# Kernel tuning notes

Hardware: AMD Instinct MI355X
Metric: run time of the kernel (lower is better)

## Reference

```python
import jax, jax.numpy as jnp
import numpy as np

N = 50000
E = 800000
IN = 128
HID = 32
H1 = 8
H2 = 4
OUT = 64
D1 = HID * H1  # 256
D2 = HID * H2  # 128
NEG_SLOPE = 0.2


def _lin(key, fin, fout):
    k1, k2 = jax.random.split(key)
    s = 1.0 / np.sqrt(fin)
    W = jax.random.uniform(k1, (fin, fout), minval=-s, maxval=s, dtype=jnp.float32)
    b = jax.random.uniform(k2, (fout,), minval=-s, maxval=s, dtype=jnp.float32)
    return W, b


def setup_inputs() -> dict:
    key = jax.random.key(0)
    ks = jax.random.split(key, 24)
    x = jax.random.normal(ks[0], (N, IN), dtype=jnp.float32)
    edge_index = jax.random.randint(ks[1], (2, E), 0, N, dtype=jnp.int64)
    W_tr, b_tr = _lin(ks[2], IN, D1)
    # GAT1: D1 -> HID per head, H1 heads (concat)
    W1, _ = _lin(ks[3], D1, H1 * HID)
    as1 = jax.random.normal(ks[4], (H1, HID), dtype=jnp.float32) * 0.1
    ad1 = jax.random.normal(ks[5], (H1, HID), dtype=jnp.float32) * 0.1
    b1 = jnp.zeros((H1 * HID,), dtype=jnp.float32)
    # GRU1: h_dim=D1, h_in_dim=D1
    Wr1, br1 = _lin(ks[6], 2 * D1, D1)
    Wz1, bz1 = _lin(ks[7], 2 * D1, D1)
    Wh1, bh1 = _lin(ks[8], 2 * D1, D1)
    Wp2, bp2 = _lin(ks[9], D1, D2)
    # GAT2: D1 -> HID per head, H2 heads
    W2, _ = _lin(ks[10], D1, H2 * HID)
    as2 = jax.random.normal(ks[11], (H2, HID), dtype=jnp.float32) * 0.1
    ad2 = jax.random.normal(ks[12], (H2, HID), dtype=jnp.float32) * 0.1
    b2 = jnp.zeros((H2 * HID,), dtype=jnp.float32)
    # GRU2: h_dim=D2, h_in_dim=D2
    Wr2, br2 = _lin(ks[13], 2 * D2, D2)
    Wz2, bz2 = _lin(ks[14], 2 * D2, D2)
    Wh2, bh2 = _lin(ks[15], 2 * D2, D2)
    Wp3, bp3 = _lin(ks[16], D2, OUT)
    # GAT3: D2 -> OUT, 1 head
    W3, _ = _lin(ks[17], D2, OUT)
    as3 = jax.random.normal(ks[18], (1, OUT), dtype=jnp.float32) * 0.1
    ad3 = jax.random.normal(ks[19], (1, OUT), dtype=jnp.float32) * 0.1
    b3 = jnp.zeros((OUT,), dtype=jnp.float32)
    # GRU3
    Wr3, br3 = _lin(ks[20], 2 * OUT, OUT)
    Wz3, bz3 = _lin(ks[21], 2 * OUT, OUT)
    Wh3, bh3 = _lin(ks[22], 2 * OUT, OUT)
    return dict(x=x, edge_index=edge_index, W_tr=W_tr, b_tr=b_tr,
                W1=W1, as1=as1, ad1=ad1, b1=b1, Wr1=Wr1, br1=br1, Wz1=Wz1, bz1=bz1, Wh1=Wh1, bh1=bh1,
                Wp2=Wp2, bp2=bp2, W2=W2, as2=as2, ad2=ad2, b2=b2, Wr2=Wr2, br2=br2, Wz2=Wz2, bz2=bz2, Wh2=Wh2, bh2=bh2,
                Wp3=Wp3, bp3=bp3, W3=W3, as3=as3, ad3=ad3, b3=b3, Wr3=Wr3, br3=br3, Wz3=Wz3, bz3=bz3, Wh3=Wh3, bh3=bh3)


def gat_conv(x, src, dst, W, a_src, a_dst, bias, heads, out_ch):
    """PyG GATConv (concat=True, add_self_loops handled by caller, eval mode so no dropout)."""
    n = x.shape[0]
    xp = (x @ W).reshape(n, heads, out_ch)            # [N,H,C]
    alpha_s = (xp * a_src[None]).sum(-1)              # [N,H]
    alpha_d = (xp * a_dst[None]).sum(-1)              # [N,H]
    e = jax.nn.leaky_relu(alpha_s[src] + alpha_d[dst], NEG_SLOPE)  # [E,H]
    # segment softmax over incoming edges of each dst node
    emax = jax.ops.segment_max(e, dst, num_segments=n)
    e = jnp.exp(e - emax[dst])
    denom = jax.ops.segment_sum(e, dst, num_segments=n)
    alpha = e / (denom[dst] + 1e-16)                  # [E,H]
    msg = xp[src] * alpha[..., None]                  # [E,H,C]
    out = jax.ops.segment_sum(msg, dst, num_segments=n)
    return out.reshape(n, heads * out_ch) + bias


def gru_sub(h, h_in, Wr, br, Wz, bz, Wh, bh):
    a = jnp.concatenate([h, h_in], axis=1)
    r = jax.nn.sigmoid(a @ Wr + br)
    z = jax.nn.sigmoid(a @ Wz + bz)
    joined = jnp.concatenate([h, r * h_in], axis=1)
    h_hat = jnp.tanh(joined @ Wh + bh)
    return (1 - z) * h_in + z * h_hat


def reference(x, edge_index, W_tr, b_tr,
              W1, as1, ad1, b1, Wr1, br1, Wz1, bz1, Wh1, bh1,
              Wp2, bp2, W2, as2, ad2, b2, Wr2, br2, Wz2, bz2, Wh2, bh2,
              Wp3, bp3, W3, as3, ad3, b3, Wr3, br3, Wz3, bz3, Wh3, bh3):
    n = x.shape[0]
    # PyG GATConv adds self-loops by default
    loop = jnp.arange(n, dtype=edge_index.dtype)
    src = jnp.concatenate([edge_index[0], loop])
    dst = jnp.concatenate([edge_index[1], loop])

    x = x @ W_tr + b_tr                                # transform: IN -> D1
    h1 = x
    x = jax.nn.elu(gat_conv(x, src, dst, W1, as1, ad1, b1, H1, HID))
    x = gru_sub(x, h1, Wr1, br1, Wz1, bz1, Wh1, bh1)
    h2 = x
    x = jax.nn.elu(gat_conv(x, src, dst, W2, as2, ad2, b2, H2, HID))
    x = gru_sub(x, h2 @ Wp2 + bp2, Wr2, br2, Wz2, bz2, Wh2, bh2)
    h3 = x
    x = gat_conv(x, src, dst, W3, as3, ad3, b3, 1, OUT)
    x = gru_sub(x, h3 @ Wp3 + bp3, Wr3, br3, Wz3, bz3, Wh3, bh3)
    return x
```

## Files before the change

### kernel.cpp

```cpp
#include <hip/hip_runtime.h>

#define NEG_SLOPE 0.2f

typedef __attribute__((ext_vector_type(8))) short short8;
typedef __attribute__((ext_vector_type(8))) unsigned short ushort8;
typedef __attribute__((ext_vector_type(4))) float f32x4;

__device__ __forceinline__ unsigned short f2bf(float f) {
    unsigned int u = __float_as_uint(f);
    u += 0x7fff + ((u >> 16) & 1);
    return (unsigned short)(u >> 16);
}
__device__ __forceinline__ float bf2f(unsigned short s) {
    return __uint_as_float(((unsigned int)s) << 16);
}

__device__ __forceinline__ void gll16(const void* g, void* l) {
    __builtin_amdgcn_global_load_lds(
        (const __attribute__((address_space(1))) void*)g,
        (__attribute__((address_space(3))) void*)l, 16, 0, 0);
}

__global__ void conv_k(const float* __restrict__ in, unsigned short* __restrict__ out, long n)
{
    long i = ((long)blockIdx.x * blockDim.x + threadIdx.x) * 4;
    if (i >= n) return;
    float4 f = *(const float4*)&in[i];
    ushort4 o; o.x = f2bf(f.x); o.y = f2bf(f.y); o.z = f2bf(f.z); o.w = f2bf(f.w);
    *(ushort4*)&out[i] = o;
}

struct WPack {
    const float* W[15];
    unsigned short* Wc[15];
    int K[15];
    int MoS[15];
    int MoD[15];
    int off[15];
};
__global__ void convW_all(WPack p)
{
    int wi = blockIdx.y;
    int i = blockIdx.x * blockDim.x + threadIdx.x;
    int K = p.K[wi], MoS = p.MoS[wi];
    if (i >= K * MoS) return;
    int k = i / MoS, m = i % MoS;
    p.Wc[wi][((long)(k >> 3) * p.MoD[wi] + p.off[wi] + m) * 8 + (k & 7)] = f2bf(p.W[wi][i]);
}

__device__ __forceinline__ int xcd_work(int TOT) {
    int L = blockIdx.x;
    int per = (TOT + 7) >> 3;
    int wk = (L & 7) * per + (L >> 3);
    return (wk < TOT) ? wk : -1;
}

template<int BN, int MODE>
__global__ __launch_bounds__(256) void gemm_t(
    const unsigned short* __restrict__ U, int K1,
    const unsigned short* __restrict__ V, int K2,
    const unsigned short* __restrict__ Wc, const float* __restrict__ bias,
    float* __restrict__ outF, unsigned short* __restrict__ outB,
    unsigned short* __restrict__ outB2,
    const unsigned short* __restrict__ HinB, const unsigned short* __restrict__ Zb,
    const float* __restrict__ HinF, const float* __restrict__ Zf,
    int rows, int Mo)
{
    constexpr int NIF = BN / 32;
    __shared__ __align__(16) unsigned short As[8][64][8];
    __shared__ __align__(16) unsigned short Bs[8][BN][8];
    const int CB = Mo / BN;
    const int RB = (rows + 63) >> 6;
    int wk = xcd_work(CB * RB);
    if (wk < 0) return;
    const int col0 = (wk % CB) * BN;
    const int row0 = (wk / CB) * 64;
    const int K = K1 + K2;
    const int tid = threadIdx.x;
    const int l = tid & 63, w = tid >> 6;
    const int lm = l & 15, lg = l >> 4;
    const int wrow = (w >> 1) * 32;
    const int wcol = (w & 1) * (BN / 2);
    f32x4 acc[2][NIF] = {};

    for (int k0 = 0; k0 < K; k0 += 64) {
#pragma unroll
        for (int i = 0; i < 2; ++i) {
            int c = i * 256 + tid;
            int m = c & 63, g = c >> 6;
            int row = row0 + m; if (row >= rows) row = rows - 1;
            int k = k0 + g * 8;
            const unsigned short* sp = (k < K1) ? U + (long)row * K1 + k
                                                : V + (long)row * K2 + (k - K1);
            gll16(sp, &As[0][0][0] + ((i * 256 + w * 64) << 3));
        }
#pragma unroll
        for (int j = 0; j < NIF; ++j) {
            int c = j * 256 + tid;
            int n = c & (BN - 1), g = c / BN;
            gll16(Wc + ((long)((k0 >> 3) + g) * Mo + (col0 + n)) * 8,
                  &Bs[0][0][0] + ((j * 256 + w * 64) << 3));
        }
        __syncthreads();
#pragma unroll
        for (int kk = 0; kk < 2; ++kk) {
            short8 a[2], b[NIF];
#pragma unroll
            for (int mi = 0; mi < 2; ++mi)
                a[mi] = *(const short8*)&As[kk * 4 + lg][wrow + mi * 16 + lm][0];
#pragma unroll
            for (int ni = 0; ni < NIF; ++ni)
                b[ni] = *(const short8*)&Bs[kk * 4 + lg][wcol + ni * 16 + lm][0];
#pragma unroll
            for (int mi = 0; mi < 2; ++mi)
#pragma unroll
                for (int ni = 0; ni < NIF; ++ni)
                    acc[mi][ni] = __builtin_amdgcn_mfma_f32_16x16x32_bf16(a[mi], b[ni], acc[mi][ni], 0, 0, 0);
        }
        __syncthreads();
    }

    const int halfMo = Mo >> 1;
#pragma unroll
    for (int mi = 0; mi < 2; ++mi) {
        int rbase = row0 + wrow + mi * 16 + lg * 4;
#pragma unroll
        for (int r = 0; r < 4; ++r) {
            int row = rbase + r;
            if (row >= rows) continue;
#pragma unroll
            for (int ni = 0; ni < NIF; ++ni) {
                int col = col0 + wcol + ni * 16 + lm;
                float v = acc[mi][ni][r];
                if (MODE == 0) {
                    v += (bias ? bias[col] : 0.f);
                    long idx = (long)row * Mo + col;
                    if (outF) outF[idx] = v;
                    if (outB) outB[idx] = f2bf(v);
                } else if (MODE == 3) {
                    v += bias[col];
                    long idx = (long)row * Mo + col;
                    float z = bf2f(Zb[idx]);
                    float o = (1.f - z) * bf2f(HinB[idx]) + z * tanhf(v);
                    outB[idx] = f2bf(o);
                } else if (MODE == 5) {
                    v += bias[col];
                    long idx = (long)row * Mo + col;
                    float z = Zf[idx];
                    float o = (1.f - z) * HinF[idx] + z * tanhf(v);
                    outF[idx] = o;
                } else {
                    if (col < halfMo) {
                        v += bias[col];
                        long idx = (long)row * halfMo + col;
                        if (outF) outF[idx] = v;
                        outB[idx] = f2bf(v);
                    } else {
                        outB2[(long)row * halfMo + (col - halfMo)] = f2bf(v);
                    }
                }
            }
        }
    }
}

template<int FP>
__global__ __launch_bounds__(256) void gemm_rz(
    const unsigned short* __restrict__ U, int K1,
    const unsigned short* __restrict__ V, int K2,
    const unsigned short* __restrict__ Wrc, const unsigned short* __restrict__ Wzc,
    const float* __restrict__ br, const float* __restrict__ bz,
    const unsigned short* __restrict__ HinB, const float* __restrict__ HinF,
    unsigned short* __restrict__ RHb,
    unsigned short* __restrict__ ZoutB, float* __restrict__ ZoutF,
    int rows, int Mo)
{
    __shared__ __align__(16) unsigned short As[8][64][8];
    __shared__ __align__(16) unsigned short Br[8][64][8];
    __shared__ __align__(16) unsigned short Bz[8][64][8];
    const int CB = Mo >> 6;
    const int RB = (rows + 63) >> 6;
    int wk = xcd_work(CB * RB);
    if (wk < 0) return;
    const int col0 = (wk % CB) * 64;
    const int row0 = (wk / CB) * 64;
    const int K = K1 + K2;
    const int tid = threadIdx.x;
    const int l = tid & 63, w = tid >> 6;
    const int lm = l & 15, lg = l >> 4;
    const int wrow = (w >> 1) * 32;
    const int wcol = (w & 1) * 32;
    f32x4 accr[2][2] = {}, accz[2][2] = {};

    for (int k0 = 0; k0 < K; k0 += 64) {
#pragma unroll
        for (int i = 0; i < 2; ++i) {
            int c = i * 256 + tid;
            int m = c & 63, g = c >> 6;
            int row = row0 + m; if (row >= rows) row = rows - 1;
            int k = k0 + g * 8;
            const unsigned short* sp = (k < K1) ? U + (long)row * K1 + k
                                                : V + (long)row * K2 + (k - K1);
            gll16(sp, &As[0][0][0] + ((i * 256 + w * 64) << 3));
        }
#pragma unroll
        for (int j = 0; j < 2; ++j) {
            int c = j * 256 + tid;
            int n = c & 63, g = c >> 6;
            long base = ((long)((k0 >> 3) + g) * Mo + (col0 + n)) * 8;
            gll16(Wrc + base, &Br[0][0][0] + ((j * 256 + w * 64) << 3));
            gll16(Wzc + base, &Bz[0][0][0] + ((j * 256 + w * 64) << 3));
        }
        __syncthreads();
#pragma unroll
        for (int kk = 0; kk < 2; ++kk) {
            short8 a[2], brv[2], bzv[2];
#pragma unroll
            for (int mi = 0; mi < 2; ++mi)
                a[mi] = *(const short8*)&As[kk * 4 + lg][wrow + mi * 16 + lm][0];
#pragma unroll
            for (int ni = 0; ni < 2; ++ni) {
                brv[ni] = *(const short8*)&Br[kk * 4 + lg][wcol + ni * 16 + lm][0];
                bzv[ni] = *(const short8*)&Bz[kk * 4 + lg][wcol + ni * 16 + lm][0];
            }
#pragma unroll
            for (int mi = 0; mi < 2; ++mi)
#pragma unroll
                for (int ni = 0; ni < 2; ++ni) {
                    accr[mi][ni] = __builtin_amdgcn_mfma_f32_16x16x32_bf16(a[mi], brv[ni], accr[mi][ni], 0, 0, 0);
                    accz[mi][ni] = __builtin_amdgcn_mfma_f32_16x16x32_bf16(a[mi], bzv[ni], accz[mi][ni], 0, 0, 0);
                }
        }
        __syncthreads();
    }

#pragma unroll
    for (int mi = 0; mi < 2; ++mi) {
        int rbase = row0 + wrow + mi * 16 + lg * 4;
#pragma unroll
        for (int r = 0; r < 4; ++r) {
            int row = rbase + r;
            if (row >= rows) continue;
#pragma unroll
            for (int ni = 0; ni < 2; ++ni) {
                int col = col0 + wcol + ni * 16 + lm;
                long idx = (long)row * Mo + col;
                float rv = 1.f / (1.f + __expf(-(accr[mi][ni][r] + br[col])));
                float zv = 1.f / (1.f + __expf(-(accz[mi][ni][r] + bz[col])));
                float hin = FP ? HinF[idx] : bf2f(HinB[idx]);
                RHb[idx] = f2bf(rv * hin);
                if (FP) ZoutF[idx] = zv;
                else    ZoutB[idx] = f2bf(zv);
            }
        }
    }
}

__global__ void alpha_b(const unsigned short* __restrict__ XPb,
                        const float* __restrict__ a_s, const float* __restrict__ a_d,
                        float* __restrict__ AS, float* __restrict__ AD,
                        int Nn, int H, int C)
{
    int i = blockIdx.x * blockDim.x + threadIdx.x;
    if (i >= Nn * H) return;
    int n = i / H, h = i % H;
    const unsigned short* xp = &XPb[(long)n * H * C + (long)h * C];
    float ss = 0.f, sd = 0.f;
    for (int c = 0; c < C; ++c) {
        float v = bf2f(xp[c]);
        ss += v * a_s[h * C + c];
        sd += v * a_d[h * C + c];
    }
    AS[i] = ss; AD[i] = sd;
}

__global__ void count_k(const int* __restrict__ dst, int E, int* __restrict__ cnt)
{
    int e = blockIdx.x * blockDim.x + threadIdx.x;
    if (e < E) atomicAdd(&cnt[dst[e]], 1);
}

__global__ __launch_bounds__(1024) void scan_k(const int* __restrict__ cnt, int Nn,
                                               int* __restrict__ off)
{
    __shared__ int part[1024];
    int tid = threadIdx.x;
    int chunk = (Nn + 1023) / 1024;
    int b = tid * chunk;
    int e = b + chunk; if (e > Nn) e = Nn; if (b > Nn) b = Nn;
    int s = 0;
    for (int i = b; i < e; ++i) s += cnt[i];
    part[tid] = s;
    __syncthreads();
    for (int d = 1; d < 1024; d <<= 1) {
        int v = (tid >= d) ? part[tid - d] : 0;
        __syncthreads();
        part[tid] += v;
        __syncthreads();
    }
    int run = tid ? part[tid - 1] : 0;
    for (int i = b; i < e; ++i) { off[i] = run; run += cnt[i]; }
    if (tid == 1023) off[Nn] = part[1023];
}

__global__ void scatter_k(const int* __restrict__ src, const int* __restrict__ dst, int E,
                          const int* __restrict__ off, int* __restrict__ cur,
                          int* __restrict__ csr_src)
{
    int e = blockIdx.x * blockDim.x + threadIdx.x;
    if (e < E) {
        int d = dst[e];
        int p = atomicAdd(&cur[d], 1);
        csr_src[off[d] + p] = src[e];
    }
}

__global__ void gat_gather_b(const int* __restrict__ off, const int* __restrict__ csr_src,
                             const unsigned short* __restrict__ XPb,
                             const float* __restrict__ AS, const float* __restrict__ AD,
                             const float* __restrict__ bias,
                             unsigned short* __restrict__ Gout,
                             int Nn, int H, int C, int do_elu)
{
    const int D = H * C;
    const int lpn = D >> 3;
    const int npw = 64 / lpn;
    int lane = threadIdx.x & 63;
    long wave = ((long)blockIdx.x * blockDim.x + threadIdx.x) >> 6;
    int sub = lane / lpn;
    int cl = lane % lpn;
    long n = wave * npw + sub;
    if (n >= Nn) return;
    int j = cl * 8;
    int h = j / C;
    float ad = AD[n * H + h];
    float v = AS[n * H + h] + ad;
    v = v > 0.f ? v : NEG_SLOPE * v;
    float w = __expf(v);
    float den = w;
    float acc[8];
    {
        ushort8 xv = *(const ushort8*)&XPb[(long)n * D + j];
#pragma unroll
        for (int q = 0; q < 8; ++q) acc[q] = w * bf2f(xv[q]);
    }
    int b0 = off[n], b1 = off[n + 1];
    int i = b0;
    for (; i + 4 <= b1; i += 4) {
        int s0 = csr_src[i + 0];
        int s1 = csr_src[i + 1];
        int s2 = csr_src[i + 2];
        int s3 = csr_src[i + 3];
        float v0 = AS[s0 * H + h] + ad;
        float v1 = AS[s1 * H + h] + ad;
        float v2 = AS[s2 * H + h] + ad;
        float v3 = AS[s3 * H + h] + ad;
        v0 = v0 > 0.f ? v0 : NEG_SLOPE * v0;
        v1 = v1 > 0.f ? v1 : NEG_SLOPE * v1;
        v2 = v2 > 0.f ? v2 : NEG_SLOPE * v2;
        v3 = v3 > 0.f ? v3 : NEG_SLOPE * v3;
        float w0 = __expf(v0), w1 = __expf(v1), w2 = __expf(v2), w3 = __expf(v3);
        den += (w0 + w1) + (w2 + w3);
        ushort8 x0 = *(const ushort8*)&XPb[(long)s0 * D + j];
        ushort8 x1 = *(const ushort8*)&XPb[(long)s1 * D + j];
        ushort8 x2 = *(const ushort8*)&XPb[(long)s2 * D + j];
        ushort8 x3 = *(const ushort8*)&XPb[(long)s3 * D + j];
#pragma unroll
        for (int q = 0; q < 8; ++q)
            acc[q] += w0 * bf2f(x0[q]) + w1 * bf2f(x1[q]) + w2 * bf2f(x2[q]) + w3 * bf2f(x3[q]);
    }
    for (; i < b1; ++i) {
        int s = csr_src[i];
        v = AS[s * H + h] + ad;
        v = v > 0.f ? v : NEG_SLOPE * v;
        w = __expf(v);
        den += w;
        ushort8 xv = *(const ushort8*)&XPb[(long)s * D + j];
#pragma unroll
        for (int q = 0; q < 8; ++q) acc[q] += w * bf2f(xv[q]);
    }
    float inv = 1.f / (den + 1e-16f);
    ushort8 ov;
#pragma unroll
    for (int q = 0; q < 8; ++q) {
        float o = acc[q] * inv + bias[j + q];
        if (do_elu) o = o > 0.f ? o : expm1f(o);
        ov[q] = f2bf(o);
    }
    *(ushort8*)&Gout[(long)n * D + j] = ov;
}

static inline int pad8(int t) { return ((t + 7) / 8) * 8; }
static inline int gblocks(int rows, int Mo, int BN) {
    return pad8((Mo / BN) * ((rows + 63) >> 6));
}

static inline void launch_gather(const int* ioff, const int* csr,
                                 const unsigned short* xp, const float* AS, const float* AD,
                                 const float* bias, unsigned short* gout,
                                 int Nn, int H, int C, int elu, hipStream_t stream)
{
    int D = H * C;
    int lpn = D >> 3;
    int npw = 64 / lpn;
    long waves = (Nn + npw - 1) / npw;
    int blocks = (int)((waves * 64 + 255) / 256);
    gat_gather_b<<<blocks, 256, 0, stream>>>(ioff, csr, xp, AS, AD, bias, gout, Nn, H, C, elu);
}

extern "C" void kernel_launch(void* const* d_in, const int* in_sizes, int n_in,
                              void* d_out, int out_size, void* d_ws, size_t ws_size,
                              hipStream_t stream)
{
    const float* x    = (const float*)d_in[0];
    const int*   ei   = (const int*)  d_in[1];
    const float* W_tr = (const float*)d_in[2];
    const float* b_tr = (const float*)d_in[3];
    const float* W1   = (const float*)d_in[4];
    const float* as1  = (const float*)d_in[5];
    const float* ad1  = (const float*)d_in[6];
    const float* b1   = (const float*)d_in[7];
    const float* Wr1  = (const float*)d_in[8];
    const float* br1  = (const float*)d_in[9];
    const float* Wz1  = (const float*)d_in[10];
    const float* bz1  = (const float*)d_in[11];
    const float* Wh1  = (const float*)d_in[12];
    const float* bh1  = (const float*)d_in[13];
    const float* Wp2  = (const float*)d_in[14];
    const float* bp2  = (const float*)d_in[15];
    const float* W2   = (const float*)d_in[16];
    const float* as2  = (const float*)d_in[17];
    const float* ad2  = (const float*)d_in[18];
    const float* b2   = (const float*)d_in[19];
    const float* Wr2  = (const float*)d_in[20];
    const float* br2  = (const float*)d_in[21];
    const float* Wz2  = (const float*)d_in[22];
    const float* bz2  = (const float*)d_in[23];
    const float* Wh2  = (const float*)d_in[24];
    const float* bh2  = (const float*)d_in[25];
    const float* Wp3  = (const float*)d_in[26];
    const float* bp3  = (const float*)d_in[27];
    const float* W3   = (const float*)d_in[28];
    const float* as3  = (const float*)d_in[29];
    const float* ad3  = (const float*)d_in[30];
    const float* b3   = (const float*)d_in[31];
    const float* Wr3  = (const float*)d_in[32];
    const float* br3  = (const float*)d_in[33];
    const float* Wz3  = (const float*)d_in[34];
    const float* bz3  = (const float*)d_in[35];
    const float* Wh3  = (const float*)d_in[36];
    const float* bh3  = (const float*)d_in[37];

    const int Nn = in_sizes[0] / 128;
    const int E  = in_sizes[1] / 2;
    const int* srcp = ei;
    const int* dstp = ei + E;

    float* AS  = (float*)d_ws;
    float* AD  = AS + (size_t)Nn * 8;
    float* H3f = AD + (size_t)Nn * 8;
    float* Z3f = H3f + (size_t)Nn * 64;
    unsigned short* X0b  = (unsigned short*)(Z3f + (size_t)Nn * 64);
    unsigned short* XPb  = X0b + (size_t)Nn * 256;
    unsigned short* Gb   = XPb + (size_t)Nn * 256;
    unsigned short* RHb  = Gb  + (size_t)Nn * 256;
    unsigned short* HINb = RHb + (size_t)Nn * 256;
    unsigned short* Zb   = HINb + (size_t)Nn * 128;
    unsigned short* wpool = Zb + (size_t)Nn * 256;
    unsigned short* Wtrc   = wpool;
    unsigned short* W1c    = Wtrc   + 128 * 256;
    unsigned short* Wr1c   = W1c    + 256 * 256;
    unsigned short* Wz1c   = Wr1c   + 512 * 256;
    unsigned short* Wh1c   = Wz1c   + 512 * 256;
    unsigned short* Wp2W2c = Wh1c   + 512 * 256;
    unsigned short* Wr2c   = Wp2W2c + 256 * 256;
    unsigned short* Wz2c   = Wr2c   + 256 * 128;
    unsigned short* Wh2c   = Wz2c   + 256 * 128;
    unsigned short* Wp3W3c = Wh2c   + 256 * 128;
    unsigned short* Wr3c   = Wp3W3c + 128 * 128;
    unsigned short* Wz3c   = Wr3c   + 128 * 64;
    unsigned short* Wh3c   = Wz3c   + 128 * 64;
    int* ioff = (int*)(((size_t)(Wh3c + 128 * 64) + 15) & ~(size_t)15);
    int* cnt  = ioff + (Nn + 1);
    int* cur  = cnt + Nn;
    int* csr  = cur + Nn;

    dim3 blk(256);

    {
        WPack p;
        const float* Ws[15]     = {W_tr, W1, Wr1, Wz1, Wh1,
                                   Wp2, W2, Wr2, Wz2, Wh2,
                                   Wp3, W3, Wr3, Wz3, Wh3};
        unsigned short* Wcs[15] = {Wtrc, W1c, Wr1c, Wz1c, Wh1c,
                                   Wp2W2c, Wp2W2c, Wr2c, Wz2c, Wh2c,
                                   Wp3W3c, Wp3W3c, Wr3c, Wz3c, Wh3c};
        int Ks[15]   = {128, 256, 512, 512, 512, 256, 256, 256, 256, 256, 128, 128, 128, 128, 128};
        int MoSs[15] = {256, 256, 256, 256, 256, 128, 128, 128, 128, 128, 64, 64, 64, 64, 64};
        int MoDs[15] = {256, 256, 256, 256, 256, 256, 256, 128, 128, 128, 128, 128, 64, 64, 64};
        int offs[15] = {0, 0, 0, 0, 0, 0, 128, 0, 0, 0, 0, 64, 0, 0, 0};
        for (int i = 0; i < 15; ++i) {
            p.W[i] = Ws[i]; p.Wc[i] = Wcs[i]; p.K[i] = Ks[i];
            p.MoS[i] = MoSs[i]; p.MoD[i] = MoDs[i]; p.off[i] = offs[i];
        }
        convW_all<<<dim3((512 * 256 + 255) / 256, 15), blk, 0, stream>>>(p);
    }

    hipMemsetAsync(cnt, 0, (size_t)Nn * 4, stream);
    hipMemsetAsync(cur, 0, (size_t)Nn * 4, stream);
    count_k<<<(E + 255) / 256, blk, 0, stream>>>(dstp, E, cnt);
    scan_k<<<1, 1024, 0, stream>>>(cnt, Nn, ioff);
    scatter_k<<<(E + 255) / 256, blk, 0, stream>>>(srcp, dstp, E, ioff, cur, csr);

    unsigned short* xb = Gb;
    conv_k<<<(int)(((long)Nn * 128 / 4 + 255) / 256), blk, 0, stream>>>(x, xb, (long)Nn * 128);
    gemm_t<128,0><<<gblocks(Nn, 256, 128), blk, 0, stream>>>(
        xb, 128, nullptr, 0, Wtrc, b_tr, nullptr, X0b, nullptr,
        nullptr, nullptr, nullptr, nullptr, Nn, 256);

    gemm_t<128,0><<<gblocks(Nn, 256, 128), blk, 0, stream>>>(
        X0b, 256, nullptr, 0, W1c, nullptr, nullptr, XPb, nullptr,
        nullptr, nullptr, nullptr, nullptr, Nn, 256);
    alpha_b<<<(Nn * 8 + 255) / 256, blk, 0, stream>>>(XPb, as1, ad1, AS, AD, Nn, 8, 32);
    launch_gather(ioff, csr, XPb, AS, AD, b1, Gb, Nn, 8, 32, 1, stream);
    gemm_rz<0><<<gblocks(Nn, 256, 64), blk, 0, stream>>>(
        Gb, 256, X0b, 256, Wr1c, Wz1c, br1, bz1, X0b, nullptr, RHb, Zb, nullptr, Nn, 256);
    gemm_t<128,3><<<gblocks(Nn, 256, 128), blk, 0, stream>>>(
        Gb, 256, RHb, 256, Wh1c, bh1, nullptr, XPb, nullptr,
        X0b, Zb, nullptr, nullptr, Nn, 256);

    gemm_t<128,4><<<gblocks(Nn, 256, 128), blk, 0, stream>>>(
        XPb, 256, nullptr, 0, Wp2W2c, bp2, nullptr, HINb, X0b,
        nullptr, nullptr, nullptr, nullptr, Nn, 256);
    alpha_b<<<(Nn * 4 + 255) / 256, blk, 0, stream>>>(X0b, as2, ad2, AS, AD, Nn, 4, 32);
    launch_gather(ioff, csr, X0b, AS, AD, b2, Gb, Nn, 4, 32, 1, stream);
    gemm_rz<0><<<gblocks(Nn, 128, 64), blk, 0, stream>>>(
        Gb, 128, HINb, 128, Wr2c, Wz2c, br2, bz2, HINb, nullptr, RHb, Zb, nullptr, Nn, 128);
    gemm_t<128,3><<<gblocks(Nn, 128, 128), blk, 0, stream>>>(
        Gb, 128, RHb, 128, Wh2c, bh2, nullptr, X0b, nullptr,
        HINb, Zb, nullptr, nullptr, Nn, 128);

    unsigned short* H3b  = HINb;
    unsigned short* XP3b = HINb + (size_t)Nn * 64;
    gemm_t<128,4><<<gblocks(Nn, 128, 128), blk, 0, stream>>>(
        X0b, 128, nullptr, 0, Wp3W3c, bp3, H3f, H3b, XP3b,
        nullptr, nullptr, nullptr, nullptr, Nn, 128);
    alpha_b<<<(Nn + 255) / 256, blk, 0, stream>>>(XP3b, as3, ad3, AS, AD, Nn, 1, 64);
    launch_gather(ioff, csr, XP3b, AS, AD, b3, Gb, Nn, 1, 64, 0, stream);
    gemm_rz<1><<<gblocks(Nn, 64, 64), blk, 0, stream>>>(
        Gb, 64, H3b, 64, Wr3c, Wz3c, br3, bz3, nullptr, H3f, RHb, nullptr, Z3f, Nn, 64);
    gemm_t<64,5><<<gblocks(Nn, 64, 64), blk, 0, stream>>>(
        Gb, 64, RHb, 64, Wh3c, bh3, (float*)d_out, nullptr, nullptr,
        nullptr, nullptr, H3f, Z3f, Nn, 64);
}
```

Measured before the change: 656.2 us.

## Split GAT gather into 32-column feature slices with 16 nodes per wave

Changes the GAT neighbor-gather mapping so each block handles a 32-column slice of the feature dimension for 64 nodes. Each wave covers 16 nodes with 4 lanes each, instead of one node spanning up to 32 lanes. Adjacent blocks in launch order work on the same node block but different slices, so concurrent blocks re-read the same CSR indices and rows, which may improve cache locality and load balance across nodes with different degrees. In exchange, edge indices and attention scores are re-read once per slice, and per-lane loops follow different node degrees, which can cause divergence within a wave.

```diff
diff --git a/kernel.cpp b/kernel.cpp
--- a/kernel.cpp
+++ b/kernel.cpp
@@ -315,24 +315,23 @@
     }
 }
 
-__global__ void gat_gather_b(const int* __restrict__ off, const int* __restrict__ csr_src,
+template<int SLICES>
+__global__ void gat_gather_s(const int* __restrict__ off, const int* __restrict__ csr_src,
                              const unsigned short* __restrict__ XPb,
                              const float* __restrict__ AS, const float* __restrict__ AD,
                              const float* __restrict__ bias,
                              unsigned short* __restrict__ Gout,
                              int Nn, int H, int C, int do_elu)
 {
-    const int D = H * C;
-    const int lpn = D >> 3;
-    const int npw = 64 / lpn;
-    int lane = threadIdx.x & 63;
-    long wave = ((long)blockIdx.x * blockDim.x + threadIdx.x) >> 6;
-    int sub = lane / lpn;
-    int cl = lane % lpn;
-    long n = wave * npw + sub;
+    const int D = SLICES * 32;
+    const int slice = blockIdx.x % SLICES;
+    const int nodeblk = blockIdx.x / SLICES;
+    const int tid = threadIdx.x;
+    const int waveid = tid >> 6, lane = tid & 63;
+    const long n = ((long)nodeblk * 4 + waveid) * 16 + (lane >> 2);
     if (n >= Nn) return;
-    int j = cl * 8;
-    int h = j / C;
+    const int j = (slice * 4 + (lane & 3)) * 8;
+    const int h = j / C;
     float ad = AD[n * H + h];
     float v = AS[n * H + h] + ad;
     v = v > 0.f ? v : NEG_SLOPE * v;
@@ -401,11 +400,15 @@
                                  int Nn, int H, int C, int elu, hipStream_t stream)
 {
     int D = H * C;
-    int lpn = D >> 3;
-    int npw = 64 / lpn;
-    long waves = (Nn + npw - 1) / npw;
-    int blocks = (int)((waves * 64 + 255) / 256);
-    gat_gather_b<<<blocks, 256, 0, stream>>>(ioff, csr, xp, AS, AD, bias, gout, Nn, H, C, elu);
+    int slices = D / 32;
+    int nodeblks = (Nn + 63) / 64;
+    int blocks = nodeblks * slices;
+    if (slices == 8)
+        gat_gather_s<8><<<blocks, 256, 0, stream>>>(ioff, csr, xp, AS, AD, bias, gout, Nn, H, C, elu);
+    else if (slices == 4)
+        gat_gather_s<4><<<blocks, 256, 0, stream>>>(ioff, csr, xp, AS, AD, bias, gout, Nn, H, C, elu);
+    else
+        gat_gather_s<2><<<blocks, 256, 0, stream>>>(ioff, csr, xp, AS, AD, bias, gout, Nn, H, C, elu);
 }
 
 extern "C" void kernel_launch(void* const* d_in, const int* in_sizes, int n_in,
```

Measured after the change: 736.5 us. +12.2%, slower.
